# Optimization experiments

Hardware: AMD Instinct MI355X
Metric: run time of the kernel (lower is better)

Reference implementation:

```python
import jax, jax.numpy as jnp
import numpy as np

N, E, F_IN, F_EDGE, HID, OUT = 100000, 1600000, 128, 8, 128, 2
BN_EPS = 1e-5


def setup_inputs() -> dict:
    key = jax.random.key(0)
    ks = jax.random.split(key, 16)
    rn = lambda k, shape, s=0.05: jax.random.normal(k, shape, jnp.float32) * s
    return {
        "x": jax.random.normal(ks[0], (N, F_IN), jnp.float32),
        "edge_attr": jax.random.uniform(ks[1], (E, F_EDGE), dtype=jnp.float32),
        "edge_index": jax.random.randint(ks[2], (2, E), 0, N, jnp.int32),
        # edge MLP: Linear(F_EDGE, HID) -> ReLU -> Linear(HID, 1) -> Sigmoid
        "ew1_w": rn(ks[3], (F_EDGE, HID)), "ew1_b": jnp.zeros((HID,), jnp.float32),
        "ew2_w": rn(ks[4], (HID, 1)), "ew2_b": jnp.zeros((1,), jnp.float32),
        # SAGEConv layers: lin_l (on aggregated neighbors, with bias) + lin_r (root)
        "w1_l": rn(ks[5], (F_IN, HID)), "b1_l": jnp.zeros((HID,), jnp.float32), "w1_r": rn(ks[6], (F_IN, HID)),
        "w2_l": rn(ks[7], (HID, HID)), "b2_l": jnp.zeros((HID,), jnp.float32), "w2_r": rn(ks[8], (HID, HID)),
        "w3_l": rn(ks[9], (HID, OUT)), "b3_l": jnp.zeros((OUT,), jnp.float32), "w3_r": rn(ks[10], (HID, OUT)),
        # BatchNorm1d (eval mode: running stats)
        "bn1_g": jnp.ones((HID,), jnp.float32), "bn1_b": jnp.zeros((HID,), jnp.float32),
        "bn1_m": rn(ks[11], (HID,), 0.01), "bn1_v": jnp.ones((HID,), jnp.float32),
        "bn2_g": jnp.ones((HID,), jnp.float32), "bn2_b": jnp.zeros((HID,), jnp.float32),
        "bn2_m": rn(ks[12], (HID,), 0.01), "bn2_v": jnp.ones((HID,), jnp.float32),
    }


def _sage(x, src, dst, ew, w_l, b_l, w_r):
    # PyG SAGEConv(aggr='mean'): msg = x[src] * edge_weight, mean over incoming edges at dst
    msg = x[src] * ew[:, None]                                  # [E, F]
    s = jax.ops.segment_sum(msg, dst, num_segments=N)           # [N, F]
    deg = jax.ops.segment_sum(jnp.ones((src.shape[0],), x.dtype), dst, num_segments=N)
    agg = s / jnp.maximum(deg, 1.0)[:, None]
    return agg @ w_l + b_l + x @ w_r


def _bn_eval(h, g, b, m, v):
    return (h - m) * jax.lax.rsqrt(v + BN_EPS) * g + b


def reference(x, edge_attr, edge_index,
              ew1_w, ew1_b, ew2_w, ew2_b,
              w1_l, b1_l, w1_r, w2_l, b2_l, w2_r, w3_l, b3_l, w3_r,
              bn1_g, bn1_b, bn1_m, bn1_v, bn2_g, bn2_b, bn2_m, bn2_v):
    src, dst = edge_index[0], edge_index[1]
    # per-edge scalar weight from small MLP
    ew = jax.nn.sigmoid(jax.nn.relu(edge_attr @ ew1_w + ew1_b) @ ew2_w + ew2_b).reshape(-1)
    h = _sage(x, src, dst, ew, w1_l, b1_l, w1_r)
    h = jax.nn.relu(_bn_eval(h, bn1_g, bn1_b, bn1_m, bn1_v))    # dropout no-op in eval
    h = _sage(h, src, dst, ew, w2_l, b2_l, w2_r)
    h = jax.nn.relu(_bn_eval(h, bn2_g, bn2_b, bn2_m, bn2_v))
    return _sage(h, src, dst, ew, w3_l, b3_l, w3_r)
```

## Files before the change

kernel.cpp:

```cpp
#include <hip/hip_runtime.h>
#include <math.h>

#define N_NODES 100000
#define N_EDGES 1600000
#define F_INF   128
#define HIDF    128

#define MLP_BLOCKS  2048
#define CAST_BLOCKS 12500
#define WP_BASE     (CAST_BLOCKS + MLP_BLOCKS)
#define FRONT_GRID  (WP_BASE + 256)

typedef __attribute__((ext_vector_type(8)))  short short8;
typedef __attribute__((ext_vector_type(16))) float floatx16;

__device__ __forceinline__ unsigned short f2bf(float f) {
    unsigned u = __float_as_uint(f);
    return (unsigned short)((u + 0x7FFFu + ((u >> 16) & 1u)) >> 16);
}
__device__ __forceinline__ float bf2f(unsigned short h) {
    return __uint_as_float((unsigned)h << 16);
}

__global__ __launch_bounds__(256) void k_front(
        const float* __restrict__ x,
        unsigned short* __restrict__ xbHi, unsigned short* __restrict__ xbLo,
        const int* __restrict__ dst, int* __restrict__ deg,
        unsigned char* __restrict__ rank,
        const float* __restrict__ ea,
        const float* __restrict__ mw1, const float* __restrict__ mb1,
        const float* __restrict__ mw2, const float* __restrict__ mb2,
        float* __restrict__ ew,
        const float* __restrict__ w1l, const float* __restrict__ w1r,
        short* __restrict__ W1hi, short* __restrict__ W1lo,
        const float* __restrict__ w2l, const float* __restrict__ w2r,
        short* __restrict__ W2hi, short* __restrict__ W2lo) {
    const int bid = blockIdx.x;

    if (bid >= WP_BASE) {
        const int wb  = bid - WP_BASE;
        const int idx = (wb & 127) * 256 + threadIdx.x;
        const float* Wl = (wb < 128) ? w1l : w2l;
        const float* Wr = (wb < 128) ? w1r : w2r;
        short* Whi = (wb < 128) ? W1hi : W2hi;
        short* Wlo = (wb < 128) ? W1lo : W2lo;
        const int j  = idx & 7;
        const int L  = (idx >> 3) & 63;
        const int cb = (idx >> 9) & 3;
        const int kb = (idx >> 11);
        const int k  = kb * 16 + (L >> 5) * 8 + j;
        const int n  = cb * 32 + (L & 31);
        const float a = (k < 128) ? Wl[k * 128 + n] : Wr[(k - 128) * 128 + n];
        const unsigned short hb = f2bf(a);
        Whi[idx] = (short)hb;
        Wlo[idx] = (short)f2bf(a - bf2f(hb));
        return;
    }

    const bool is_mlp = ((bid % 7) == 3) && (bid < 7 * MLP_BLOCKS);
    if (!is_mlp) {
        const int c   = (bid < 4) ? 0 : min(MLP_BLOCKS, (bid - 4) / 7 + 1);
        const int gid = (bid - c) * 256 + (int)threadIdx.x;
        const int i   = gid * 4;
        const float4 v = *(const float4*)(x + i);
        ushort4 h, l;
        h.x = f2bf(v.x); l.x = f2bf(v.x - bf2f(h.x));
        h.y = f2bf(v.y); l.y = f2bf(v.y - bf2f(h.y));
        h.z = f2bf(v.z); l.z = f2bf(v.z - bf2f(h.z));
        h.w = f2bf(v.w); l.w = f2bf(v.w - bf2f(h.w));
        *(ushort4*)(xbHi + i) = h;
        *(ushort4*)(xbLo + i) = l;
        if ((gid & 1) == 0) {
            const int e = gid >> 1;
            rank[e] = (unsigned char)atomicAdd(&deg[dst[e]], 1);
        }
        return;
    }

    const int lane = threadIdx.x & 63;
    const int cl   = lane & 31;
    const int half = lane >> 5;
    const int wid  = (bid / 7) * 4 + ((int)threadIdx.x >> 6);
    const int nw   = MLP_BLOCKS * 4;

    short8 bw[4];
    float  w2c[4];
#pragma unroll
    for (int cb = 0; cb < 4; ++cb) {
        const int n = cb * 32 + cl;
        short8 b;
        if (half == 0) {
#pragma unroll
            for (int j = 0; j < 8; ++j) b[j] = (short)f2bf(mw1[j * 128 + n]);
        } else {
            b[0] = (short)f2bf(mb1[n]);
#pragma unroll
            for (int j = 1; j < 8; ++j) b[j] = 0;
        }
        bw[cb] = b;
        w2c[cb] = mw2[n];
    }
    short8 Abias;
    Abias[0] = (short)0x3F80;
#pragma unroll
    for (int j = 1; j < 8; ++j) Abias[j] = 0;

    floatx16 czero;
#pragma unroll
    for (int r = 0; r < 16; ++r) czero[r] = 0.f;

    const float bias2 = mb2[0];

    for (int e0 = wid * 32; e0 < N_EDGES; e0 += nw * 32) {
        short8 Ah;
        if (half == 0) {
            const float4 a0 = *(const float4*)(ea + (size_t)(e0 + cl) * 8);
            const float4 a1 = *(const float4*)(ea + (size_t)(e0 + cl) * 8 + 4);
            Ah[0] = (short)f2bf(a0.x); Ah[1] = (short)f2bf(a0.y);
            Ah[2] = (short)f2bf(a0.z); Ah[3] = (short)f2bf(a0.w);
            Ah[4] = (short)f2bf(a1.x); Ah[5] = (short)f2bf(a1.y);
            Ah[6] = (short)f2bf(a1.z); Ah[7] = (short)f2bf(a1.w);
        } else {
            Ah = Abias;
        }

        float z[16];
#pragma unroll
        for (int r = 0; r < 16; ++r) z[r] = 0.f;

#pragma unroll
        for (int cb = 0; cb < 4; ++cb) {
            floatx16 acc = __builtin_amdgcn_mfma_f32_32x32x16_bf16(Ah, bw[cb], czero, 0, 0, 0);
#pragma unroll
            for (int r = 0; r < 16; ++r)
                z[r] = fmaf(fmaxf(acc[r], 0.f), w2c[cb], z[r]);
        }

#pragma unroll
        for (int m = 1; m <= 16; m <<= 1) {
#pragma unroll
            for (int r = 0; r < 16; ++r) z[r] += __shfl_xor(z[r], m, 64);
        }

        float zz = z[0];
#pragma unroll
        for (int r = 1; r < 16; ++r) zz = (cl == r) ? z[r] : zz;
        if (cl < 16) {
            const int row = (cl & 3) + 8 * (cl >> 2) + 4 * half;
            ew[e0 + row] = 1.f / (1.f + __expf(-(zz + bias2)));
        }
    }
}

__global__ void k_scan1(const int* __restrict__ deg, int* __restrict__ incl,
                        int* __restrict__ bsum) {
    __shared__ int sm[1024];
    const int tid = threadIdx.x;
    const int gi  = blockIdx.x * 1024 + tid;
    int v = (gi < N_NODES) ? deg[gi] : 0;
    sm[tid] = v;
    __syncthreads();
    for (int off = 1; off < 1024; off <<= 1) {
        int t = (tid >= off) ? sm[tid - off] : 0;
        __syncthreads();
        sm[tid] += t;
        __syncthreads();
    }
    if (gi < N_NODES) incl[gi] = sm[tid];
    if (tid == 1023) bsum[blockIdx.x] = sm[1023];
}

__global__ void k_scan23(const int* __restrict__ incl, const int* __restrict__ bsum,
                         int* __restrict__ rowptr, int nb) {
    __shared__ int sm[128];
    const int tid = threadIdx.x;
    int v = 0;
    if (tid < 128) {
        v = (tid < nb) ? bsum[tid] : 0;
        sm[tid] = v;
    }
    __syncthreads();
    for (int off = 1; off < 128; off <<= 1) {
        int t = 0;
        if (tid < 128 && tid >= off) t = sm[tid - off];
        __syncthreads();
        if (tid < 128) sm[tid] += t;
        __syncthreads();
    }
    if (tid < 128) sm[tid] -= v;
    __syncthreads();
    const int i = blockIdx.x * 256 + tid;
    if (i < N_NODES) rowptr[i + 1] = sm[i >> 10] + incl[i];
    if (i == 0) rowptr[0] = 0;
}

__global__ void k_fill(const int* __restrict__ src, const int* __restrict__ dst,
                       const float* __restrict__ ew, const int* __restrict__ rowptr,
                       const unsigned char* __restrict__ rank,
                       unsigned* __restrict__ cw) {
    int e = blockIdx.x * 256 + threadIdx.x;
    if (e < N_EDGES) {
        int d   = dst[e];
        int pos = rowptr[d] + (int)rank[e];
        unsigned wb = (unsigned)f2bf(ew[e]) & 0x7FFFu;
        cw[pos] = ((unsigned)src[e] << 15) | wb;
    }
}

__global__ __launch_bounds__(256) void k_agg16(
        const unsigned short* __restrict__ xb, const int* __restrict__ rowptr,
        const unsigned* __restrict__ cw,
        unsigned short* __restrict__ aggHi, unsigned short* __restrict__ aggLo) {
    const int lane = threadIdx.x & 63;
    const int half = lane >> 5;
    const int cl   = lane & 31;
    const int node = blockIdx.x * (blockDim.x >> 6) + (threadIdx.x >> 6);
    if (node >= N_NODES) return;
    const int s = rowptr[node], e = rowptr[node + 1];
    float a0 = 0.f, a1 = 0.f, a2 = 0.f, a3 = 0.f;

    for (int j0 = s; j0 < e; j0 += 8) {
        int ss[4]; float ww[4];
#pragma unroll
        for (int u = 0; u < 4; ++u) {
            const int j  = j0 + 2 * u + half;
            const int jc = min(j, e - 1);
            const unsigned p = cw[jc];
            ss[u] = (int)(p >> 15);
            ww[u] = (j < e) ? __uint_as_float((p & 0x7FFFu) << 16) : 0.f;
        }
        uint2 g[4];
#pragma unroll
        for (int u = 0; u < 4; ++u)
            g[u] = *(const uint2*)(xb + (size_t)ss[u] * 128 + cl * 4);
#pragma unroll
        for (int u = 0; u < 4; ++u) {
            const float f0 = __uint_as_float(g[u].x << 16);
            const float f1 = __uint_as_float(g[u].x & 0xFFFF0000u);
            const float f2 = __uint_as_float(g[u].y << 16);
            const float f3 = __uint_as_float(g[u].y & 0xFFFF0000u);
            a0 = fmaf(ww[u], f0, a0);
            a1 = fmaf(ww[u], f1, a1);
            a2 = fmaf(ww[u], f2, a2);
            a3 = fmaf(ww[u], f3, a3);
        }
    }
    a0 += __shfl_xor(a0, 32, 64);
    a1 += __shfl_xor(a1, 32, 64);
    a2 += __shfl_xor(a2, 32, 64);
    a3 += __shfl_xor(a3, 32, 64);
    if (half == 0) {
        const float inv = 1.f / fmaxf((float)(e - s), 1.f);
        a0 *= inv; a1 *= inv; a2 *= inv; a3 *= inv;
        ushort4 h, l;
        h.x = f2bf(a0); l.x = f2bf(a0 - bf2f(h.x));
        h.y = f2bf(a1); l.y = f2bf(a1 - bf2f(h.y));
        h.z = f2bf(a2); l.z = f2bf(a2 - bf2f(h.z));
        h.w = f2bf(a3); l.w = f2bf(a3 - bf2f(h.w));
        *(ushort4*)(aggHi + (size_t)node * 128 + cl * 4) = h;
        *(ushort4*)(aggLo + (size_t)node * 128 + cl * 4) = l;
    }
}

__global__ __launch_bounds__(256) void k_gemm(
    const unsigned short* __restrict__ AaggHi, const unsigned short* __restrict__ AaggLo,
    const unsigned short* __restrict__ AxHi, const unsigned short* __restrict__ AxLo,
    const short* __restrict__ Whi, const short* __restrict__ Wlo,
    const float* __restrict__ bl,
    const float* __restrict__ bng, const float* __restrict__ bnb,
    const float* __restrict__ bnm, const float* __restrict__ bnv,
    unsigned short* __restrict__ outHi, unsigned short* __restrict__ outLo) {
    __shared__ unsigned short SH[32 * 128];
    __shared__ unsigned short SL[32 * 128];
    const int tid  = threadIdx.x;
    const int lane = tid & 63;
    const int cb   = tid >> 6;
    const int rrow = lane & 31;
    const int kq   = lane >> 5;
    const int row0 = blockIdx.x * 32;

    const int sr = tid >> 3;
    const int sc = (tid & 7) * 16;
    const int s0 = sc >> 3;
    const size_t gsrc = (size_t)(row0 + sr) * 128 + sc;
    const int ld0 = sr * 128 + ((s0 + 0) ^ (sr & 15)) * 8;
    const int ld1 = sr * 128 + ((s0 + 1) ^ (sr & 15)) * 8;

    const uint4 ah0 = *(const uint4*)(AaggHi + gsrc);
    const uint4 ah1 = *(const uint4*)(AaggHi + gsrc + 8);
    const uint4 al0 = *(const uint4*)(AaggLo + gsrc);
    const uint4 al1 = *(const uint4*)(AaggLo + gsrc + 8);
    const uint4 rh0 = *(const uint4*)(AxHi + gsrc);
    const uint4 rh1 = *(const uint4*)(AxHi + gsrc + 8);
    const uint4 rl0 = *(const uint4*)(AxLo + gsrc);
    const uint4 rl1 = *(const uint4*)(AxLo + gsrc + 8);

    *(uint4*)(SH + ld0) = ah0;
    *(uint4*)(SH + ld1) = ah1;
    *(uint4*)(SL + ld0) = al0;
    *(uint4*)(SL + ld1) = al1;

    floatx16 acc;
#pragma unroll
    for (int r = 0; r < 16; ++r) acc[r] = 0.f;

    __syncthreads();

#pragma unroll
    for (int kb = 0; kb < 8; ++kb) {
        const int slot = (2 * kb + kq) ^ (rrow & 15);
        const short8 Ah = *(const short8*)(SH + rrow * 128 + slot * 8);
        const short8 Al = *(const short8*)(SL + rrow * 128 + slot * 8);
        const size_t wo = ((size_t)(kb * 4 + cb) * 64 + lane) * 8;
        const short8 wh = *(const short8*)(Whi + wo);
        const short8 wl = *(const short8*)(Wlo + wo);
        acc = __builtin_amdgcn_mfma_f32_32x32x16_bf16(Ah, wh, acc, 0, 0, 0);
        acc = __builtin_amdgcn_mfma_f32_32x32x16_bf16(Al, wh, acc, 0, 0, 0);
        acc = __builtin_amdgcn_mfma_f32_32x32x16_bf16(Ah, wl, acc, 0, 0, 0);
    }

    __syncthreads();
    *(uint4*)(SH + ld0) = rh0;
    *(uint4*)(SH + ld1) = rh1;
    *(uint4*)(SL + ld0) = rl0;
    *(uint4*)(SL + ld1) = rl1;
    __syncthreads();

#pragma unroll
    for (int kb = 0; kb < 8; ++kb) {
        const int slot = (2 * kb + kq) ^ (rrow & 15);
        const short8 Ah = *(const short8*)(SH + rrow * 128 + slot * 8);
        const short8 Al = *(const short8*)(SL + rrow * 128 + slot * 8);
        const size_t wo = ((size_t)((kb + 8) * 4 + cb) * 64 + lane) * 8;
        const short8 wh = *(const short8*)(Whi + wo);
        const short8 wl = *(const short8*)(Wlo + wo);
        acc = __builtin_amdgcn_mfma_f32_32x32x16_bf16(Ah, wh, acc, 0, 0, 0);
        acc = __builtin_amdgcn_mfma_f32_32x32x16_bf16(Al, wh, acc, 0, 0, 0);
        acc = __builtin_amdgcn_mfma_f32_32x32x16_bf16(Ah, wl, acc, 0, 0, 0);
    }

    const int c = cb * 32 + rrow;
    const float s = bng[c] * rsqrtf(bnv[c] + 1e-5f);
    const float t = (bl[c] - bnm[c]) * s + bnb[c];
#pragma unroll
    for (int r = 0; r < 16; ++r) {
        const int row = row0 + (r & 3) + 8 * (r >> 2) + 4 * kq;
        const float v = fmaxf(fmaf(acc[r], s, t), 0.f);
        const unsigned short hb = f2bf(v);
        outHi[(size_t)row * 128 + c] = hb;
        outLo[(size_t)row * 128 + c] = f2bf(v - bf2f(hb));
    }
}

__global__ void k_lin3(const unsigned short* __restrict__ hHi,
                       const unsigned short* __restrict__ hLo,
                       const float* __restrict__ w3l,
                       const float* __restrict__ w3r, float* __restrict__ t4) {
    const int lane = threadIdx.x & 63;
    const int node = blockIdx.x * (blockDim.x >> 6) + (threadIdx.x >> 6);
    if (node >= N_NODES) return;
    const size_t b = (size_t)node * 128;
    const float h0 = bf2f(hHi[b + lane])      + bf2f(hLo[b + lane]);
    const float h1 = bf2f(hHi[b + 64 + lane]) + bf2f(hLo[b + 64 + lane]);
    const float2 wl0 = *(const float2*)(w3l + lane * 2);
    const float2 wl1 = *(const float2*)(w3l + (64 + lane) * 2);
    const float2 wr0 = *(const float2*)(w3r + lane * 2);
    const float2 wr1 = *(const float2*)(w3r + (64 + lane) * 2);
    float p0 = h0 * wl0.x + h1 * wl1.x;
    float p1 = h0 * wl0.y + h1 * wl1.y;
    float p2 = h0 * wr0.x + h1 * wr1.x;
    float p3 = h0 * wr0.y + h1 * wr1.y;
#pragma unroll
    for (int m = 1; m < 64; m <<= 1) {
        p0 += __shfl_xor(p0, m, 64);
        p1 += __shfl_xor(p1, m, 64);
        p2 += __shfl_xor(p2, m, 64);
        p3 += __shfl_xor(p3, m, 64);
    }
    if (lane == 0) {
        float4 o; o.x = p0; o.y = p1; o.z = p2; o.w = p3;
        *(float4*)(t4 + (size_t)node * 4) = o;
    }
}

__global__ void k_out(const float* __restrict__ t4, const int* __restrict__ rowptr,
                      const unsigned* __restrict__ cw,
                      const float* __restrict__ b3, float* __restrict__ out) {
    const int lane = threadIdx.x & 63;
    const int node = blockIdx.x * (blockDim.x >> 6) + (threadIdx.x >> 6);
    if (node >= N_NODES) return;
    const int s = rowptr[node], e = rowptr[node + 1];
    float a0 = 0.f, a1 = 0.f;
    for (int j = s + lane; j < e; j += 64) {
        const unsigned p = cw[j];
        const int   sr = (int)(p >> 15);
        const float w  = __uint_as_float((p & 0x7FFFu) << 16);
        float2 t = *(const float2*)(t4 + (size_t)sr * 4);
        a0 += w * t.x; a1 += w * t.y;
    }
#pragma unroll
    for (int m = 1; m < 64; m <<= 1) {
        a0 += __shfl_xor(a0, m, 64);
        a1 += __shfl_xor(a1, m, 64);
    }
    if (lane == 0) {
        float inv = 1.f / fmaxf((float)(e - s), 1.f);
        float2 o;
        o.x = a0 * inv + b3[0] + t4[(size_t)node * 4 + 2];
        o.y = a1 * inv + b3[1] + t4[(size_t)node * 4 + 3];
        *(float2*)(out + (size_t)node * 2) = o;
    }
}

extern "C" void kernel_launch(void* const* d_in, const int* in_sizes, int n_in,
                              void* d_out, int out_size, void* d_ws, size_t ws_size,
                              hipStream_t stream) {
    const float* x    = (const float*)d_in[0];
    const float* ea   = (const float*)d_in[1];
    const int*   ei   = (const int*)d_in[2];
    const float* ew1w = (const float*)d_in[3];
    const float* ew1b = (const float*)d_in[4];
    const float* ew2w = (const float*)d_in[5];
    const float* ew2b = (const float*)d_in[6];
    const float* w1l  = (const float*)d_in[7];
    const float* b1l  = (const float*)d_in[8];
    const float* w1r  = (const float*)d_in[9];
    const float* w2l  = (const float*)d_in[10];
    const float* b2l  = (const float*)d_in[11];
    const float* w2r  = (const float*)d_in[12];
    const float* w3l  = (const float*)d_in[13];
    const float* b3l  = (const float*)d_in[14];
    const float* w3r  = (const float*)d_in[15];
    const float* bn1g = (const float*)d_in[16];
    const float* bn1b = (const float*)d_in[17];
    const float* bn1m = (const float*)d_in[18];
    const float* bn1v = (const float*)d_in[19];
    const float* bn2g = (const float*)d_in[20];
    const float* bn2b = (const float*)d_in[21];
    const float* bn2m = (const float*)d_in[22];
    const float* bn2v = (const float*)d_in[23];

    const int* src = ei;
    const int* dst = ei + N_EDGES;
    float* out = (float*)d_out;

    size_t off = 0;
    auto carve = [&](size_t bytes) -> void* {
        void* p = (char*)d_ws + off;
        off += (bytes + 255) & ~(size_t)255;
        return p;
    };
    float* ew     = (float*)carve((size_t)N_EDGES * 4);
    unsigned* cw  = (unsigned*)carve((size_t)N_EDGES * 4);
    unsigned char* rank = (unsigned char*)carve((size_t)N_EDGES);
    int*   rowptr = (int*)carve((size_t)(N_NODES + 1) * 4);
    int*   deg    = (int*)carve((size_t)N_NODES * 4);
    int*   bsum   = (int*)carve(128 * 4);
    int*   incl   = (int*)carve((size_t)N_NODES * 4);
    float* t4     = (float*)carve((size_t)N_NODES * 4 * 4);
    short* W1hi   = (short*)carve(32768 * 2);
    short* W1lo   = (short*)carve(32768 * 2);
    short* W2hi   = (short*)carve(32768 * 2);
    short* W2lo   = (short*)carve(32768 * 2);
    unsigned short* xbHi  = (unsigned short*)carve((size_t)N_NODES * 128 * 2);
    unsigned short* xbLo  = (unsigned short*)carve((size_t)N_NODES * 128 * 2);
    unsigned short* aggHi = (unsigned short*)carve((size_t)N_NODES * 128 * 2);
    unsigned short* aggLo = (unsigned short*)carve((size_t)N_NODES * 128 * 2);
    unsigned short* hHi   = (unsigned short*)carve((size_t)N_NODES * 128 * 2);
    unsigned short* hLo   = (unsigned short*)carve((size_t)N_NODES * 128 * 2);
    unsigned short* hBhi  = (unsigned short*)carve((size_t)N_NODES * 128 * 2);
    unsigned short* hBlo  = (unsigned short*)carve((size_t)N_NODES * 128 * 2);
    (void)ws_size; (void)n_in; (void)in_sizes; (void)out_size;

    hipMemsetAsync(deg, 0, (size_t)N_NODES * 4, stream);

    const int EB = (N_EDGES + 255) / 256;
    const int NB_SCAN = (N_NODES + 1023) / 1024;
    const int NWB = (N_NODES + 3) / 4;
    const int GB = N_NODES / 32;

    k_front<<<FRONT_GRID, 256, 0, stream>>>(
        x, xbHi, xbLo, dst, deg, rank,
        ea, ew1w, ew1b, ew2w, ew2b, ew,
        w1l, w1r, W1hi, W1lo, w2l, w2r, W2hi, W2lo);
    k_scan1<<<NB_SCAN, 1024, 0, stream>>>(deg, incl, bsum);
    k_scan23<<<(N_NODES + 255) / 256, 256, 0, stream>>>(incl, bsum, rowptr, NB_SCAN);
    k_fill<<<EB, 256, 0, stream>>>(src, dst, ew, rowptr, rank, cw);

    k_agg16<<<NWB, 256, 0, stream>>>(xbHi, rowptr, cw, aggHi, aggLo);
    k_gemm<<<GB, 256, 0, stream>>>(aggHi, aggLo, xbHi, xbLo, W1hi, W1lo, b1l,
                                   bn1g, bn1b, bn1m, bn1v, hHi, hLo);
    k_agg16<<<NWB, 256, 0, stream>>>(hHi, rowptr, cw, aggHi, aggLo);
    k_gemm<<<GB, 256, 0, stream>>>(aggHi, aggLo, hHi, hLo, W2hi, W2lo, b2l,
                                   bn2g, bn2b, bn2m, bn2v, hBhi, hBlo);
    k_lin3<<<NWB, 256, 0, stream>>>(hBhi, hBlo, w3l, w3r, t4);
    k_out<<<NWB, 256, 0, stream>>>(t4, rowptr, cw, b3l, out);
}
```

Baseline: 525.7 us.

## Use LDS-binned degree counting and fuse layer-3 projection into second GEMM

Replaces global atomic degree counting with per-strip, per-range LDS histogram blocks that write partial degrees and pack per-strip offsets, so the CSR fill combines strip offset and local rank. The memset and the global atomics on deg go away, but each block rescans its whole strip of dst. Separately, the second SAGE GEMM now keeps its BN+ReLU output in LDS and runs the 128->4 layer-3 projection with MFMA in the same kernel. This removes the hB round trip through global memory and the separate k_lin3 launch. The cost is extra LDS traffic, barriers and a single-wave tail in which most MFMA lanes are zero.

```diff
diff --git a/kernel.cpp b/kernel.cpp
--- a/kernel.cpp
+++ b/kernel.cpp
@@ -6,10 +6,16 @@
 #define F_INF   128
 #define HIDF    128
 
+#define S_STRIPS   4
+#define STRIP_E    (N_EDGES / S_STRIPS)
+#define DEG_RB     64
+#define DEG_BLOCKS (S_STRIPS * DEG_RB)
+#define RANGE_SZ   1563
+
 #define MLP_BLOCKS  2048
 #define CAST_BLOCKS 12500
 #define WP_BASE     (CAST_BLOCKS + MLP_BLOCKS)
-#define FRONT_GRID  (WP_BASE + 256)
+#define FRONT_GRID  (DEG_BLOCKS + WP_BASE + 256)
 
 typedef __attribute__((ext_vector_type(8)))  short short8;
 typedef __attribute__((ext_vector_type(16))) float floatx16;
@@ -25,7 +31,7 @@
 __global__ __launch_bounds__(256) void k_front(
         const float* __restrict__ x,
         unsigned short* __restrict__ xbHi, unsigned short* __restrict__ xbLo,
-        const int* __restrict__ dst, int* __restrict__ deg,
+        const int* __restrict__ dst, int* __restrict__ pdeg,
         unsigned char* __restrict__ rank,
         const float* __restrict__ ea,
         const float* __restrict__ mw1, const float* __restrict__ mb1,
@@ -35,10 +41,41 @@
         short* __restrict__ W1hi, short* __restrict__ W1lo,
         const float* __restrict__ w2l, const float* __restrict__ w2r,
         short* __restrict__ W2hi, short* __restrict__ W2lo) {
+    __shared__ int bins[RANGE_SZ];
     const int bid = blockIdx.x;
 
-    if (bid >= WP_BASE) {
-        const int wb  = bid - WP_BASE;
+    if (bid < DEG_BLOCKS) {
+        const int sid = bid >> 6;
+        const int rng = bid & 63;
+        const int lo  = rng * RANGE_SZ;
+        const int cnt = min(RANGE_SZ, N_NODES - lo);
+        for (int i = threadIdx.x; i < cnt; i += 256) bins[i] = 0;
+        __syncthreads();
+        const uint4* d4 = (const uint4*)dst;
+        const int q0 = sid * (STRIP_E / 4);
+        const int q1 = q0 + STRIP_E / 4;
+        for (int q = q0 + (int)threadIdx.x; q < q1; q += 256) {
+            const uint4 v = d4[q];
+            const int e = q * 4;
+            unsigned r;
+            r = v.x - (unsigned)lo;
+            if (r < (unsigned)cnt) rank[e]     = (unsigned char)atomicAdd(&bins[r], 1);
+            r = v.y - (unsigned)lo;
+            if (r < (unsigned)cnt) rank[e + 1] = (unsigned char)atomicAdd(&bins[r], 1);
+            r = v.z - (unsigned)lo;
+            if (r < (unsigned)cnt) rank[e + 2] = (unsigned char)atomicAdd(&bins[r], 1);
+            r = v.w - (unsigned)lo;
+            if (r < (unsigned)cnt) rank[e + 3] = (unsigned char)atomicAdd(&bins[r], 1);
+        }
+        __syncthreads();
+        for (int i = threadIdx.x; i < cnt; i += 256)
+            pdeg[sid * N_NODES + lo + i] = bins[i];
+        return;
+    }
+
+    const int b2 = bid - DEG_BLOCKS;
+    if (b2 >= WP_BASE) {
+        const int wb  = b2 - WP_BASE;
         const int idx = (wb & 127) * 256 + threadIdx.x;
         const float* Wl = (wb < 128) ? w1l : w2l;
         const float* Wr = (wb < 128) ? w1r : w2r;
@@ -57,10 +94,10 @@
         return;
     }
 
-    const bool is_mlp = ((bid % 7) == 3) && (bid < 7 * MLP_BLOCKS);
+    const bool is_mlp = ((b2 % 7) == 3) && (b2 < 7 * MLP_BLOCKS);
     if (!is_mlp) {
-        const int c   = (bid < 4) ? 0 : min(MLP_BLOCKS, (bid - 4) / 7 + 1);
-        const int gid = (bid - c) * 256 + (int)threadIdx.x;
+        const int c   = (b2 < 4) ? 0 : min(MLP_BLOCKS, (b2 - 4) / 7 + 1);
+        const int gid = (b2 - c) * 256 + (int)threadIdx.x;
         const int i   = gid * 4;
         const float4 v = *(const float4*)(x + i);
         ushort4 h, l;
@@ -70,17 +107,13 @@
         h.w = f2bf(v.w); l.w = f2bf(v.w - bf2f(h.w));
         *(ushort4*)(xbHi + i) = h;
         *(ushort4*)(xbLo + i) = l;
-        if ((gid & 1) == 0) {
-            const int e = gid >> 1;
-            rank[e] = (unsigned char)atomicAdd(&deg[dst[e]], 1);
-        }
         return;
     }
 
     const int lane = threadIdx.x & 63;
     const int cl   = lane & 31;
     const int half = lane >> 5;
-    const int wid  = (bid / 7) * 4 + ((int)threadIdx.x >> 6);
+    const int wid  = (b2 / 7) * 4 + ((int)threadIdx.x >> 6);
     const int nw   = MLP_BLOCKS * 4;
 
     short8 bw[4];
@@ -152,12 +185,21 @@
     }
 }
 
-__global__ void k_scan1(const int* __restrict__ deg, int* __restrict__ incl,
-                        int* __restrict__ bsum) {
+__global__ void k_scan1(const int* __restrict__ pdeg, int* __restrict__ incl,
+                        int* __restrict__ bsum, unsigned* __restrict__ sOff) {
     __shared__ int sm[1024];
     const int tid = threadIdx.x;
     const int gi  = blockIdx.x * 1024 + tid;
-    int v = (gi < N_NODES) ? deg[gi] : 0;
+    int p0 = 0, p1 = 0, p2 = 0, p3 = 0;
+    if (gi < N_NODES) {
+        p0 = pdeg[gi];
+        p1 = pdeg[N_NODES + gi];
+        p2 = pdeg[2 * N_NODES + gi];
+        p3 = pdeg[3 * N_NODES + gi];
+        sOff[gi] = ((unsigned)p0 << 8) | ((unsigned)(p0 + p1) << 16)
+                 | ((unsigned)(p0 + p1 + p2) << 24);
+    }
+    int v = p0 + p1 + p2 + p3;
     sm[tid] = v;
     __syncthreads();
     for (int off = 1; off < 1024; off <<= 1) {
@@ -197,11 +239,13 @@
 __global__ void k_fill(const int* __restrict__ src, const int* __restrict__ dst,
                        const float* __restrict__ ew, const int* __restrict__ rowptr,
                        const unsigned char* __restrict__ rank,
+                       const unsigned* __restrict__ sOff,
                        unsigned* __restrict__ cw) {
     int e = blockIdx.x * 256 + threadIdx.x;
     if (e < N_EDGES) {
         int d   = dst[e];
-        int pos = rowptr[d] + (int)rank[e];
+        int sid = e / STRIP_E;
+        int pos = rowptr[d] + (int)((sOff[d] >> (sid * 8)) & 0xFFu) + (int)rank[e];
         unsigned wb = (unsigned)f2bf(ew[e]) & 0x7FFFu;
         cw[pos] = ((unsigned)src[e] << 15) | wb;
     }
@@ -352,34 +396,134 @@
     }
 }
 
-__global__ void k_lin3(const unsigned short* __restrict__ hHi,
-                       const unsigned short* __restrict__ hLo,
-                       const float* __restrict__ w3l,
-                       const float* __restrict__ w3r, float* __restrict__ t4) {
-    const int lane = threadIdx.x & 63;
-    const int node = blockIdx.x * (blockDim.x >> 6) + (threadIdx.x >> 6);
-    if (node >= N_NODES) return;
-    const size_t b = (size_t)node * 128;
-    const float h0 = bf2f(hHi[b + lane])      + bf2f(hLo[b + lane]);
-    const float h1 = bf2f(hHi[b + 64 + lane]) + bf2f(hLo[b + 64 + lane]);
-    const float2 wl0 = *(const float2*)(w3l + lane * 2);
-    const float2 wl1 = *(const float2*)(w3l + (64 + lane) * 2);
-    const float2 wr0 = *(const float2*)(w3r + lane * 2);
-    const float2 wr1 = *(const float2*)(w3r + (64 + lane) * 2);
-    float p0 = h0 * wl0.x + h1 * wl1.x;
-    float p1 = h0 * wl0.y + h1 * wl1.y;
-    float p2 = h0 * wr0.x + h1 * wr1.x;
-    float p3 = h0 * wr0.y + h1 * wr1.y;
-#pragma unroll
-    for (int m = 1; m < 64; m <<= 1) {
-        p0 += __shfl_xor(p0, m, 64);
-        p1 += __shfl_xor(p1, m, 64);
-        p2 += __shfl_xor(p2, m, 64);
-        p3 += __shfl_xor(p3, m, 64);
-    }
-    if (lane == 0) {
-        float4 o; o.x = p0; o.y = p1; o.z = p2; o.w = p3;
-        *(float4*)(t4 + (size_t)node * 4) = o;
+__global__ __launch_bounds__(256) void k_gemm2(
+    const unsigned short* __restrict__ AaggHi, const unsigned short* __restrict__ AaggLo,
+    const unsigned short* __restrict__ AxHi, const unsigned short* __restrict__ AxLo,
+    const short* __restrict__ Whi, const short* __restrict__ Wlo,
+    const float* __restrict__ bl,
+    const float* __restrict__ bng, const float* __restrict__ bnb,
+    const float* __restrict__ bnm, const float* __restrict__ bnv,
+    const float* __restrict__ w3l, const float* __restrict__ w3r,
+    float* __restrict__ t4) {
+    __shared__ unsigned short SH[32 * 128];
+    __shared__ unsigned short SL[32 * 128];
+    const int tid  = threadIdx.x;
+    const int lane = tid & 63;
+    const int cb   = tid >> 6;
+    const int rrow = lane & 31;
+    const int kq   = lane >> 5;
+    const int row0 = blockIdx.x * 32;
+
+    const int sr = tid >> 3;
+    const int sc = (tid & 7) * 16;
+    const int s0 = sc >> 3;
+    const size_t gsrc = (size_t)(row0 + sr) * 128 + sc;
+    const int ld0 = sr * 128 + ((s0 + 0) ^ (sr & 15)) * 8;
+    const int ld1 = sr * 128 + ((s0 + 1) ^ (sr & 15)) * 8;
+
+    const uint4 ah0 = *(const uint4*)(AaggHi + gsrc);
+    const uint4 ah1 = *(const uint4*)(AaggHi + gsrc + 8);
+    const uint4 al0 = *(const uint4*)(AaggLo + gsrc);
+    const uint4 al1 = *(const uint4*)(AaggLo + gsrc + 8);
+    const uint4 rh0 = *(const uint4*)(AxHi + gsrc);
+    const uint4 rh1 = *(const uint4*)(AxHi + gsrc + 8);
+    const uint4 rl0 = *(const uint4*)(AxLo + gsrc);
+    const uint4 rl1 = *(const uint4*)(AxLo + gsrc + 8);
+
+    *(uint4*)(SH + ld0) = ah0;
+    *(uint4*)(SH + ld1) = ah1;
+    *(uint4*)(SL + ld0) = al0;
+    *(uint4*)(SL + ld1) = al1;
+
+    floatx16 acc;
+#pragma unroll
+    for (int r = 0; r < 16; ++r) acc[r] = 0.f;
+
+    __syncthreads();
+
+#pragma unroll
+    for (int kb = 0; kb < 8; ++kb) {
+        const int slot = (2 * kb + kq) ^ (rrow & 15);
+        const short8 Ah = *(const short8*)(SH + rrow * 128 + slot * 8);
+        const short8 Al = *(const short8*)(SL + rrow * 128 + slot * 8);
+        const size_t wo = ((size_t)(kb * 4 + cb) * 64 + lane) * 8;
+        const short8 wh = *(const short8*)(Whi + wo);
+        const short8 wl = *(const short8*)(Wlo + wo);
+        acc = __builtin_amdgcn_mfma_f32_32x32x16_bf16(Ah, wh, acc, 0, 0, 0);
+        acc = __builtin_amdgcn_mfma_f32_32x32x16_bf16(Al, wh, acc, 0, 0, 0);
+        acc = __builtin_amdgcn_mfma_f32_32x32x16_bf16(Ah, wl, acc, 0, 0, 0);
+    }
+
+    __syncthreads();
+    *(uint4*)(SH + ld0) = rh0;
+    *(uint4*)(SH + ld1) = rh1;
+    *(uint4*)(SL + ld0) = rl0;
+    *(uint4*)(SL + ld1) = rl1;
+    __syncthreads();
+
+#pragma unroll
+    for (int kb = 0; kb < 8; ++kb) {
+        const int slot = (2 * kb + kq) ^ (rrow & 15);
+        const short8 Ah = *(const short8*)(SH + rrow * 128 + slot * 8);
+        const short8 Al = *(const short8*)(SL + rrow * 128 + slot * 8);
+        const size_t wo = ((size_t)((kb + 8) * 4 + cb) * 64 + lane) * 8;
+        const short8 wh = *(const short8*)(Whi + wo);
+        const short8 wl = *(const short8*)(Wlo + wo);
+        acc = __builtin_amdgcn_mfma_f32_32x32x16_bf16(Ah, wh, acc, 0, 0, 0);
+        acc = __builtin_amdgcn_mfma_f32_32x32x16_bf16(Al, wh, acc, 0, 0, 0);
+        acc = __builtin_amdgcn_mfma_f32_32x32x16_bf16(Ah, wl, acc, 0, 0, 0);
+    }
+
+    const int c = cb * 32 + rrow;
+    const float s = bng[c] * rsqrtf(bnv[c] + 1e-5f);
+    const float t = (bl[c] - bnm[c]) * s + bnb[c];
+    __syncthreads();
+#pragma unroll
+    for (int r = 0; r < 16; ++r) {
+        const int rl = (r & 3) + 8 * (r >> 2) + 4 * kq;
+        const float v = fmaxf(fmaf(acc[r], s, t), 0.f);
+        const unsigned short hb = f2bf(v);
+        const int sl = ((c >> 3) ^ (rl & 15)) * 8 + (c & 7);
+        SH[rl * 128 + sl] = hb;
+        SL[rl * 128 + sl] = f2bf(v - bf2f(hb));
+    }
+    __syncthreads();
+
+    if (tid < 64) {
+        const int n = rrow;
+        floatx16 a2;
+#pragma unroll
+        for (int r = 0; r < 16; ++r) a2[r] = 0.f;
+#pragma unroll
+        for (int kb = 0; kb < 8; ++kb) {
+            const int slot = (2 * kb + kq) ^ (rrow & 15);
+            const short8 Ah = *(const short8*)(SH + rrow * 128 + slot * 8);
+            const short8 Al = *(const short8*)(SL + rrow * 128 + slot * 8);
+            short8 Bh, Bl;
+            if (n < 4) {
+#pragma unroll
+                for (int j = 0; j < 8; ++j) {
+                    const int k = kb * 16 + kq * 8 + j;
+                    const float f = (n < 2) ? w3l[k * 2 + n] : w3r[k * 2 + (n - 2)];
+                    const unsigned short hb2 = f2bf(f);
+                    Bh[j] = (short)hb2;
+                    Bl[j] = (short)f2bf(f - bf2f(hb2));
+                }
+            } else {
+#pragma unroll
+                for (int j = 0; j < 8; ++j) { Bh[j] = 0; Bl[j] = 0; }
+            }
+            a2 = __builtin_amdgcn_mfma_f32_32x32x16_bf16(Ah, Bh, a2, 0, 0, 0);
+            a2 = __builtin_amdgcn_mfma_f32_32x32x16_bf16(Al, Bh, a2, 0, 0, 0);
+            a2 = __builtin_amdgcn_mfma_f32_32x32x16_bf16(Ah, Bl, a2, 0, 0, 0);
+        }
+        if (n < 4) {
+#pragma unroll
+            for (int r = 0; r < 16; ++r) {
+                const int row = row0 + (r & 3) + 8 * (r >> 2) + 4 * kq;
+                t4[(size_t)row * 4 + n] = a2[r];
+            }
+        }
     }
 }
 
@@ -454,7 +598,8 @@
     unsigned* cw  = (unsigned*)carve((size_t)N_EDGES * 4);
     unsigned char* rank = (unsigned char*)carve((size_t)N_EDGES);
     int*   rowptr = (int*)carve((size_t)(N_NODES + 1) * 4);
-    int*   deg    = (int*)carve((size_t)N_NODES * 4);
+    int*   pdeg   = (int*)carve((size_t)S_STRIPS * N_NODES * 4);
+    unsigned* sOff = (unsigned*)carve((size_t)N_NODES * 4);
     int*   bsum   = (int*)carve(128 * 4);
     int*   incl   = (int*)carve((size_t)N_NODES * 4);
     float* t4     = (float*)carve((size_t)N_NODES * 4 * 4);
@@ -468,11 +613,7 @@
     unsigned short* aggLo = (unsigned short*)carve((size_t)N_NODES * 128 * 2);
     unsigned short* hHi   = (unsigned short*)carve((size_t)N_NODES * 128 * 2);
     unsigned short* hLo   = (unsigned short*)carve((size_t)N_NODES * 128 * 2);
-    unsigned short* hBhi  = (unsigned short*)carve((size_t)N_NODES * 128 * 2);
-    unsigned short* hBlo  = (unsigned short*)carve((size_t)N_NODES * 128 * 2);
     (void)ws_size; (void)n_in; (void)in_sizes; (void)out_size;
-
-    hipMemsetAsync(deg, 0, (size_t)N_NODES * 4, stream);
 
     const int EB = (N_EDGES + 255) / 256;
     const int NB_SCAN = (N_NODES + 1023) / 1024;
@@ -480,19 +621,18 @@
     const int GB = N_NODES / 32;
 
     k_front<<<FRONT_GRID, 256, 0, stream>>>(
-        x, xbHi, xbLo, dst, deg, rank,
+        x, xbHi, xbLo, dst, pdeg, rank,
         ea, ew1w, ew1b, ew2w, ew2b, ew,
         w1l, w1r, W1hi, W1lo, w2l, w2r, W2hi, W2lo);
-    k_scan1<<<NB_SCAN, 1024, 0, stream>>>(deg, incl, bsum);
+    k_scan1<<<NB_SCAN, 1024, 0, stream>>>(pdeg, incl, bsum, sOff);
     k_scan23<<<(N_NODES + 255) / 256, 256, 0, stream>>>(incl, bsum, rowptr, NB_SCAN);
-    k_fill<<<EB, 256, 0, stream>>>(src, dst, ew, rowptr, rank, cw);
+    k_fill<<<EB, 256, 0, stream>>>(src, dst, ew, rowptr, rank, sOff, cw);
 
     k_agg16<<<NWB, 256, 0, stream>>>(xbHi, rowptr, cw, aggHi, aggLo);
     k_gemm<<<GB, 256, 0, stream>>>(aggHi, aggLo, xbHi, xbLo, W1hi, W1lo, b1l,
                                    bn1g, bn1b, bn1m, bn1v, hHi, hLo);
     k_agg16<<<NWB, 256, 0, stream>>>(hHi, rowptr, cw, aggHi, aggLo);
-    k_gemm<<<GB, 256, 0, stream>>>(aggHi, aggLo, hHi, hLo, W2hi, W2lo, b2l,
-                                   bn2g, bn2b, bn2m, bn2v, hBhi, hBlo);
-    k_lin3<<<NWB, 256, 0, stream>>>(hBhi, hBlo, w3l, w3r, t4);
+    k_gemm2<<<GB, 256, 0, stream>>>(aggHi, aggLo, hHi, hLo, W2hi, W2lo, b2l,
+                                    bn2g, bn2b, bn2m, bn2v, w3l, w3r, t4);
     k_out<<<NWB, 256, 0, stream>>>(t4, rowptr, cw, b3l, out);
 }
```

Measured after the change: 643.0 us. +22.3%, slower.
